# Kernel tuning notes

Hardware: AMD Instinct MI355X
Metric: run time of the kernel (lower is better)

The kernel has to match this reference:

```python
import jax, jax.numpy as jnp
import numpy as np

HEAD_COUNT = 16  # original code scales by head_count ** -0.5 (not head_size)


def setup_inputs() -> dict:
    key = jax.random.key(0)
    k1, k2, k3, k4 = jax.random.split(key, 4)
    B, T, C, H = 4, 4096, 1024, 64
    x = jax.random.normal(k1, (B, T, C), dtype=jnp.float32)
    # nn.Linear(C, H, bias=False) weights, stored as (C, H) so projection is x @ W
    Wq = jax.random.normal(k2, (C, H), dtype=jnp.float32) * (C ** -0.5)
    Wk = jax.random.normal(k3, (C, H), dtype=jnp.float32) * (C ** -0.5)
    Wv = jax.random.normal(k4, (C, H), dtype=jnp.float32) * (C ** -0.5)
    return {"x": x, "Wq": Wq, "Wk": Wk, "Wv": Wv}


def reference(x, Wq, Wk, Wv):
    B, T, C = x.shape
    q = jnp.einsum('btc,ch->bth', x, Wq)  # [B,T,H]
    k = jnp.einsum('btc,ch->bth', x, Wk)
    v = jnp.einsum('btc,ch->bth', x, Wv)
    scale = HEAD_COUNT ** (-0.5)
    scores = jnp.einsum('bth,bsh->bts', q, k) * scale  # [B,T,T]
    causal = jnp.tril(jnp.ones((T, T), dtype=bool))
    scores = jnp.where(causal, scores, -jnp.inf)
    weights = jax.nn.softmax(scores, axis=-1)
    # dropout disabled (eval / rate 0) for deterministic reference
    out = jnp.einsum('bts,bsh->bth', weights, v)  # [B,T,H]
    return out
```

## Files before the change

### kernel.cpp

```cpp
#include <hip/hip_runtime.h>
#include <hip/hip_bf16.h>


typedef __attribute__((ext_vector_type(8))) short short8_t;
typedef __attribute__((ext_vector_type(4))) float f32x4;
typedef __attribute__((ext_vector_type(16))) float f32x16;

#define MFMA16(a, b, c) __builtin_amdgcn_mfma_f32_16x16x32_bf16((a), (b), (c), 0, 0, 0)
#define MFMA32(a, b, c) __builtin_amdgcn_mfma_f32_32x32x16_bf16((a), (b), (c), 0, 0, 0)

__device__ __forceinline__ unsigned short f2bf(float f) {
  union { float f; unsigned int u; } v; v.f = f;
  unsigned int u = v.u;
  u += 0x7FFFu + ((u >> 16) & 1u);
  return (unsigned short)(u >> 16);
}
__device__ __forceinline__ float bf2f(unsigned short h) {
  union { unsigned int u; float f; } v; v.u = ((unsigned int)h) << 16;
  return v.f;
}

__global__ __launch_bounds__(256) void qkv_proj(
    const float* __restrict__ x,  const float* __restrict__ Wq,
    const float* __restrict__ Wk, const float* __restrict__ Wv,
    unsigned short* __restrict__ qh, unsigned short* __restrict__ ql,
    unsigned short* __restrict__ kh, unsigned short* __restrict__ kl,
    unsigned short* __restrict__ vth, unsigned short* __restrict__ vtl)
{
  __shared__ alignas(16) unsigned short Ah[64][40];
  __shared__ alignas(16) unsigned short Al[64][40];
  __shared__ alignas(16) unsigned short Bh[192][40];
  __shared__ alignas(16) unsigned short Bl[192][40];

  const int tid  = threadIdx.x;
  const int wave = tid >> 6;
  const int lane = tid & 63;
  const int g    = lane >> 4;
  const int c    = lane & 15;
  const int m0   = blockIdx.x * 64;

  f32x4 acc[4][3];
#pragma unroll
  for (int m = 0; m < 4; ++m)
#pragma unroll
    for (int nn = 0; nn < 3; ++nn) acc[m][nn] = (f32x4){0.f, 0.f, 0.f, 0.f};

  for (int k0 = 0; k0 < 1024; k0 += 32) {
    __syncthreads();
#pragma unroll
    for (int it = 0; it < 2; ++it) {
      int chunk = tid + it * 256;
      int row = chunk >> 3, ch = chunk & 7;
      const float4 vx = *reinterpret_cast<const float4*>(
          x + (size_t)(m0 + row) * 1024 + k0 + ch * 4);
#pragma unroll
      for (int j = 0; j < 4; ++j) {
        float f = ((const float*)&vx)[j];
        unsigned short h = f2bf(f);
        Ah[row][ch * 4 + j] = h;
        Al[row][ch * 4 + j] = f2bf(f - bf2f(h));
      }
    }
    const float* const Ws[3] = {Wq, Wk, Wv};
#pragma unroll
    for (int it = 0; it < 6; ++it) {
      int chunk = tid + it * 256;
      int mat = chunk >> 9;
      int cid = chunk & 511;
      int kk = cid >> 4, ch = cid & 15;
      const float4 vw = *reinterpret_cast<const float4*>(
          Ws[mat] + (size_t)(k0 + kk) * 64 + ch * 4);
#pragma unroll
      for (int j = 0; j < 4; ++j) {
        float f = ((const float*)&vw)[j];
        unsigned short h = f2bf(f);
        int n = mat * 64 + ch * 4 + j;
        Bh[n][kk] = h;
        Bl[n][kk] = f2bf(f - bf2f(h));
      }
    }
    __syncthreads();

    short8_t a_h[4], a_l[4];
#pragma unroll
    for (int m = 0; m < 4; ++m) {
      a_h[m] = *reinterpret_cast<const short8_t*>(&Ah[m * 16 + c][g * 8]);
      a_l[m] = *reinterpret_cast<const short8_t*>(&Al[m * 16 + c][g * 8]);
    }
#pragma unroll
    for (int nn = 0; nn < 3; ++nn) {
      const int nt = wave * 3 + nn;
      short8_t b_h = *reinterpret_cast<const short8_t*>(&Bh[nt * 16 + c][g * 8]);
      short8_t b_l = *reinterpret_cast<const short8_t*>(&Bl[nt * 16 + c][g * 8]);
#pragma unroll
      for (int m = 0; m < 4; ++m) {
        acc[m][nn] = MFMA16(a_h[m], b_h, acc[m][nn]);
        acc[m][nn] = MFMA16(a_h[m], b_l, acc[m][nn]);
        acc[m][nn] = MFMA16(a_l[m], b_h, acc[m][nn]);
      }
    }
  }

#pragma unroll
  for (int m = 0; m < 4; ++m) {
#pragma unroll
    for (int nn = 0; nn < 3; ++nn) {
      const int nt  = wave * 3 + nn;
      const int mat = nt >> 2;
      const int col = (nt & 3) * 16 + c;
#pragma unroll
      for (int r = 0; r < 4; ++r) {
        float f = acc[m][nn][r];
        int row = m0 + m * 16 + g * 4 + r;
        unsigned short h = f2bf(f);
        unsigned short lo = f2bf(f - bf2f(h));
        if (mat == 0) {
          size_t idx = (size_t)row * 64 + col;
          qh[idx] = h; ql[idx] = lo;
        } else if (mat == 1) {
          size_t idx = (size_t)row * 64 + col;
          kh[idx] = h; kl[idx] = lo;
        } else {
          int bb = row >> 12, trow = row & 4095;
          size_t idx = ((size_t)(bb * 64 + col)) * 4096 + trow;
          vth[idx] = h; vtl[idx] = lo;
        }
      }
    }
  }
}

#define MASKVAL (-3.0e38f)
#define MINIT   (-1.0e30f)

__global__ __launch_bounds__(512, 2) void attn(
    const unsigned short* __restrict__ qh, const unsigned short* __restrict__ ql,
    const unsigned short* __restrict__ kh, const unsigned short* __restrict__ kl,
    const unsigned short* __restrict__ vth, const unsigned short* __restrict__ vtl,
    float* __restrict__ out)
{
  __shared__ alignas(16) unsigned char smem[147456];

  const int tid = threadIdx.x;
  const int ws  = tid >> 6;
  const int l   = tid & 63;
  const int h5  = l >> 5;
  const int l31 = l & 31;
  const int bid = blockIdx.x;
  const int bb  = bid >> 6;
  const int jt  = bid & 63;
  const int t0  = jt * 64;

  unsigned short* Kh = (unsigned short*)(smem + ws * 18432);
  unsigned short* Kl = (unsigned short*)(smem + ws * 18432 + 4096);
  unsigned short* Vh = (unsigned short*)(smem + ws * 18432 + 8192);
  unsigned short* Vl = (unsigned short*)(smem + ws * 18432 + 13312);

  const float CE = 0.36067376022224085f;

  short8_t qf_h[2][4], qf_l[2][4];
#pragma unroll
  for (int qt = 0; qt < 2; ++qt)
#pragma unroll
    for (int c = 0; c < 4; ++c) {
      size_t off = ((size_t)(bb * 4096 + t0 + qt * 32 + l31)) * 64 + c * 16 + h5 * 8;
      qf_h[qt][c] = *reinterpret_cast<const short8_t*>(qh + off);
      qf_l[qt][c] = *reinterpret_cast<const short8_t*>(ql + off);
    }

  f32x16 ot[2][2];
#pragma unroll
  for (int a = 0; a < 2; ++a)
#pragma unroll
    for (int b2 = 0; b2 < 2; ++b2)
#pragma unroll
      for (int r = 0; r < 16; ++r) ot[a][b2][r] = 0.f;
  float mreg[2] = {MINIT, MINIT};
  float lreg[2] = {0.f, 0.f};

  const int ktimax = (t0 + 63) >> 5;

  for (int kti = ws; kti <= ktimax; kti += 8) {
    const int s0 = kti * 32;

#pragma unroll
    for (int i = 0; i < 4; ++i) {
      int k2 = i * 8 + (l >> 3);
      int hh = (l & 7) * 8;
      size_t gidx = ((size_t)(bb * 4096 + s0 + k2)) * 64 + hh;
      short8_t a = *reinterpret_cast<const short8_t*>(kh + gidx);
      short8_t b2 = *reinterpret_cast<const short8_t*>(kl + gidx);
      int wo = k2 * 64 + (hh ^ ((k2 & 7) << 3));
      *reinterpret_cast<short8_t*>(Kh + wo) = a;
      *reinterpret_cast<short8_t*>(Kl + wo) = b2;
    }
#pragma unroll
    for (int i = 0; i < 4; ++i) {
      int hv = i * 16 + (l >> 2);
      int kv = (l & 3) * 8;
      size_t gidx = ((size_t)(bb * 64 + hv)) * 4096 + s0 + kv;
      short8_t a = *reinterpret_cast<const short8_t*>(vth + gidx);
      short8_t b2 = *reinterpret_cast<const short8_t*>(vtl + gidx);
      int wo = hv * 40 + kv;
      *reinterpret_cast<short8_t*>(Vh + wo) = a;
      *reinterpret_cast<short8_t*>(Vl + wo) = b2;
    }

    short8_t kf_h[4], kf_l[4];
#pragma unroll
    for (int c = 0; c < 4; ++c) {
      int ko = l31 * 64 + ((c * 16 + h5 * 8) ^ ((l31 & 7) << 3));
      kf_h[c] = *reinterpret_cast<const short8_t*>(Kh + ko);
      kf_l[c] = *reinterpret_cast<const short8_t*>(Kl + ko);
    }

    int pb0[2][4], pb1[2][4], plb0[2][4], plb1[2][4];

#pragma unroll
    for (int qt = 0; qt < 2; ++qt) {
      int (*pb)[4]  = (qt == 0) ? pb0 : pb1;
      int (*plb)[4] = (qt == 0) ? plb0 : plb1;
      if (s0 > t0 + qt * 32 + 31) {
#pragma unroll
        for (int kc = 0; kc < 2; ++kc)
#pragma unroll
          for (int d = 0; d < 4; ++d) { pb[kc][d] = 0; plb[kc][d] = 0; }
        continue;
      }

      f32x16 st;
#pragma unroll
      for (int r = 0; r < 16; ++r) st[r] = 0.f;
#pragma unroll
      for (int c = 0; c < 4; ++c) {
        st = MFMA32(kf_h[c], qf_h[qt][c], st);
        st = MFMA32(kf_h[c], qf_l[qt][c], st);
        st = MFMA32(kf_l[c], qf_h[qt][c], st);
      }

      if (s0 + 31 > t0 + qt * 32) {
        int qg = t0 + qt * 32 + l31;
#pragma unroll
        for (int r = 0; r < 16; ++r) {
          int keyg = s0 + (r & 3) + 8 * (r >> 2) + 4 * h5;
          if (keyg > qg) st[r] = MASKVAL;
        }
      }

      float pm = st[0];
#pragma unroll
      for (int r = 1; r < 16; ++r) pm = fmaxf(pm, st[r]);
      pm = fmaxf(pm, __shfl_xor(pm, 32));
      float mnew = fmaxf(mreg[qt], pm);
      float fs = __builtin_amdgcn_exp2f((mreg[qt] - mnew) * CE);
      mreg[qt] = mnew;
      lreg[qt] *= fs;
#pragma unroll
      for (int ht = 0; ht < 2; ++ht) ot[ht][qt] *= fs;

      float p[16]; float rs = 0.f;
#pragma unroll
      for (int r = 0; r < 16; ++r) {
        p[r] = __builtin_amdgcn_exp2f((st[r] - mnew) * CE);
        rs += p[r];
      }
      rs += __shfl_xor(rs, 32);
      lreg[qt] += rs;

      int w[8], wl[8], pw[8], pwl[8];
#pragma unroll
      for (int i = 0; i < 8; ++i) {
        unsigned short b0 = f2bf(p[2 * i]), b1 = f2bf(p[2 * i + 1]);
        w[i] = (int)((unsigned)b0 | ((unsigned)b1 << 16));
        float l0 = p[2 * i] - bf2f(b0), l1 = p[2 * i + 1] - bf2f(b1);
        wl[i] = (int)((unsigned)f2bf(l0) | ((unsigned)f2bf(l1) << 16));
      }
#pragma unroll
      for (int i = 0; i < 8; ++i) {
        pw[i]  = __shfl_xor(w[i], 32);
        pwl[i] = __shfl_xor(wl[i], 32);
      }
#pragma unroll
      for (int kc = 0; kc < 2; ++kc) {
        pb[kc][0]  = h5 ? pw[4 * kc + 2]  : w[4 * kc];
        pb[kc][1]  = h5 ? pw[4 * kc + 3]  : w[4 * kc + 1];
        pb[kc][2]  = h5 ? w[4 * kc + 2]   : pw[4 * kc];
        pb[kc][3]  = h5 ? w[4 * kc + 3]   : pw[4 * kc + 1];
        plb[kc][0] = h5 ? pwl[4 * kc + 2] : wl[4 * kc];
        plb[kc][1] = h5 ? pwl[4 * kc + 3] : wl[4 * kc + 1];
        plb[kc][2] = h5 ? wl[4 * kc + 2]  : pwl[4 * kc];
        plb[kc][3] = h5 ? wl[4 * kc + 3]  : pwl[4 * kc + 1];
      }
    }

#pragma unroll
    for (int ht = 0; ht < 2; ++ht)
#pragma unroll
      for (int kc = 0; kc < 2; ++kc) {
        int vo = (ht * 32 + l31) * 40 + kc * 16 + h5 * 8;
        short8_t vfh = *reinterpret_cast<const short8_t*>(Vh + vo);
        short8_t vfl = *reinterpret_cast<const short8_t*>(Vl + vo);
#pragma unroll
        for (int qt = 0; qt < 2; ++qt) {
          union { int d[4]; short8_t s; } u1, u2;
#pragma unroll
          for (int d = 0; d < 4; ++d) {
            u1.d[d] = (qt == 0) ? pb0[kc][d] : pb1[kc][d];
            u2.d[d] = (qt == 0) ? plb0[kc][d] : plb1[kc][d];
          }
          ot[ht][qt] = MFMA32(vfh, u1.s, ot[ht][qt]);
          ot[ht][qt] = MFMA32(vfl, u1.s, ot[ht][qt]);
          ot[ht][qt] = MFMA32(vfh, u2.s, ot[ht][qt]);
        }
      }
  }

  __syncthreads();
  float* OT = (float*)smem;
  float* ML = (float*)(smem + 137216);
#pragma unroll
  for (int ht = 0; ht < 2; ++ht)
#pragma unroll
    for (int qt = 0; qt < 2; ++qt)
#pragma unroll
      for (int r = 0; r < 16; ++r) {
        int h = ht * 32 + (r & 3) + 8 * (r >> 2) + 4 * h5;
        int q = qt * 32 + l31;
        OT[(ws * 64 + h) * 67 + q] = ot[ht][qt][r];
      }
  if (l < 32) {
#pragma unroll
    for (int qt = 0; qt < 2; ++qt) {
      int q = qt * 32 + l31;
      ML[(ws * 64 + q) * 2]     = mreg[qt];
      ML[(ws * 64 + q) * 2 + 1] = lreg[qt];
    }
  }
  __syncthreads();

  {
    const int h = tid & 63;
    const int qg = tid >> 6;
#pragma unroll
    for (int i = 0; i < 8; ++i) {
      int q = qg * 8 + i;
      float M = ML[q * 2];
#pragma unroll
      for (int s = 1; s < 8; ++s) M = fmaxf(M, ML[(s * 64 + q) * 2]);
      float L = 0.f, acc2 = 0.f;
#pragma unroll
      for (int s = 0; s < 8; ++s) {
        float wgt = __builtin_amdgcn_exp2f((ML[(s * 64 + q) * 2] - M) * CE);
        L    += wgt * ML[(s * 64 + q) * 2 + 1];
        acc2 += wgt * OT[(s * 64 + h) * 67 + q];
      }
      out[((size_t)bb * 4096 + t0 + q) * 64 + h] = acc2 / L;
    }
  }
}

extern "C" void kernel_launch(void* const* d_in, const int* in_sizes, int n_in,
                              void* d_out, int out_size, void* d_ws, size_t ws_size,
                              hipStream_t stream) {
  const float* x  = (const float*)d_in[0];
  const float* Wq = (const float*)d_in[1];
  const float* Wk = (const float*)d_in[2];
  const float* Wv = (const float*)d_in[3];
  float* out = (float*)d_out;

  const size_t NE = (size_t)16384 * 64;
  unsigned short* qh  = (unsigned short*)d_ws;
  unsigned short* ql  = qh + NE;
  unsigned short* kh  = ql + NE;
  unsigned short* kl  = kh + NE;
  unsigned short* vth = kl + NE;
  unsigned short* vtl = vth + NE;

  qkv_proj<<<256, 256, 0, stream>>>(x, Wq, Wk, Wv, qh, ql, kh, kl, vth, vtl);
  attn<<<256, 512, 0, stream>>>(qh, ql, kh, kl, vth, vtl, out);
}
```

Measured before the change: 257.0 us.

## Split causal attention into load-balanced KV slices with merge kernel, pre-split weights

```diff
diff --git a/kernel.cpp b/kernel.cpp
--- a/kernel.cpp
+++ b/kernel.cpp
@@ -20,80 +20,79 @@
   return v.f;
 }
 
+__device__ __forceinline__ size_t vtidx(int b, int t, int h) {
+  return ((((((size_t)b * 128 + (t >> 5)) * 2 + (h >> 5)) * 2 + ((t >> 4) & 1)) * 2
+           + ((t >> 3) & 1)) * 32 + (h & 31)) * 8 + (t & 7);
+}
+
+__global__ __launch_bounds__(192) void wprep(
+    const float* __restrict__ Wq, const float* __restrict__ Wk,
+    const float* __restrict__ Wv,
+    unsigned short* __restrict__ wth, unsigned short* __restrict__ wtl)
+{
+  const int n  = threadIdx.x;
+  const int kb = blockIdx.x;
+  const float* W = (n < 64) ? Wq : (n < 128) ? Wk : Wv;
+  const int cc = n & 63;
+  union { unsigned short u[8]; short8_t s; } uh, ul;
+#pragma unroll
+  for (int j = 0; j < 8; ++j) {
+    float f = W[(size_t)(kb * 8 + j) * 64 + cc];
+    unsigned short h = f2bf(f);
+    uh.u[j] = h;
+    ul.u[j] = f2bf(f - bf2f(h));
+  }
+  *reinterpret_cast<short8_t*>(wth + (size_t)n * 1024 + kb * 8) = uh.s;
+  *reinterpret_cast<short8_t*>(wtl + (size_t)n * 1024 + kb * 8) = ul.s;
+}
+
 __global__ __launch_bounds__(256) void qkv_proj(
-    const float* __restrict__ x,  const float* __restrict__ Wq,
-    const float* __restrict__ Wk, const float* __restrict__ Wv,
+    const float* __restrict__ x,
+    const unsigned short* __restrict__ wth, const unsigned short* __restrict__ wtl,
     unsigned short* __restrict__ qh, unsigned short* __restrict__ ql,
     unsigned short* __restrict__ kh, unsigned short* __restrict__ kl,
     unsigned short* __restrict__ vth, unsigned short* __restrict__ vtl)
 {
-  __shared__ alignas(16) unsigned short Ah[64][40];
-  __shared__ alignas(16) unsigned short Al[64][40];
-  __shared__ alignas(16) unsigned short Bh[192][40];
-  __shared__ alignas(16) unsigned short Bl[192][40];
-
   const int tid  = threadIdx.x;
   const int wave = tid >> 6;
   const int lane = tid & 63;
   const int g    = lane >> 4;
   const int c    = lane & 15;
-  const int m0   = blockIdx.x * 64;
-
-  f32x4 acc[4][3];
-#pragma unroll
-  for (int m = 0; m < 4; ++m)
+  const int m0   = blockIdx.x * 32;
+
+  f32x4 acc[2][3];
+#pragma unroll
+  for (int m = 0; m < 2; ++m)
 #pragma unroll
     for (int nn = 0; nn < 3; ++nn) acc[m][nn] = (f32x4){0.f, 0.f, 0.f, 0.f};
 
   for (int k0 = 0; k0 < 1024; k0 += 32) {
-    __syncthreads();
-#pragma unroll
-    for (int it = 0; it < 2; ++it) {
-      int chunk = tid + it * 256;
-      int row = chunk >> 3, ch = chunk & 7;
-      const float4 vx = *reinterpret_cast<const float4*>(
-          x + (size_t)(m0 + row) * 1024 + k0 + ch * 4);
+    short8_t a_h[2], a_l[2];
+#pragma unroll
+    for (int m = 0; m < 2; ++m) {
+      const float* xp = x + (size_t)(m0 + m * 16 + c) * 1024 + k0 + g * 8;
+      const float4 f0 = *reinterpret_cast<const float4*>(xp);
+      const float4 f1 = *reinterpret_cast<const float4*>(xp + 4);
+      union { unsigned short u[8]; short8_t s; } uh, ul;
 #pragma unroll
       for (int j = 0; j < 4; ++j) {
-        float f = ((const float*)&vx)[j];
-        unsigned short h = f2bf(f);
-        Ah[row][ch * 4 + j] = h;
-        Al[row][ch * 4 + j] = f2bf(f - bf2f(h));
-      }
-    }
-    const float* const Ws[3] = {Wq, Wk, Wv};
-#pragma unroll
-    for (int it = 0; it < 6; ++it) {
-      int chunk = tid + it * 256;
-      int mat = chunk >> 9;
-      int cid = chunk & 511;
-      int kk = cid >> 4, ch = cid & 15;
-      const float4 vw = *reinterpret_cast<const float4*>(
-          Ws[mat] + (size_t)(k0 + kk) * 64 + ch * 4);
-#pragma unroll
-      for (int j = 0; j < 4; ++j) {
-        float f = ((const float*)&vw)[j];
-        unsigned short h = f2bf(f);
-        int n = mat * 64 + ch * 4 + j;
-        Bh[n][kk] = h;
-        Bl[n][kk] = f2bf(f - bf2f(h));
-      }
-    }
-    __syncthreads();
-
-    short8_t a_h[4], a_l[4];
-#pragma unroll
-    for (int m = 0; m < 4; ++m) {
-      a_h[m] = *reinterpret_cast<const short8_t*>(&Ah[m * 16 + c][g * 8]);
-      a_l[m] = *reinterpret_cast<const short8_t*>(&Al[m * 16 + c][g * 8]);
+        float fa = ((const float*)&f0)[j];
+        unsigned short ha = f2bf(fa);
+        uh.u[j] = ha; ul.u[j] = f2bf(fa - bf2f(ha));
+        float fb = ((const float*)&f1)[j];
+        unsigned short hb = f2bf(fb);
+        uh.u[4 + j] = hb; ul.u[4 + j] = f2bf(fb - bf2f(hb));
+      }
+      a_h[m] = uh.s; a_l[m] = ul.s;
     }
 #pragma unroll
     for (int nn = 0; nn < 3; ++nn) {
       const int nt = wave * 3 + nn;
-      short8_t b_h = *reinterpret_cast<const short8_t*>(&Bh[nt * 16 + c][g * 8]);
-      short8_t b_l = *reinterpret_cast<const short8_t*>(&Bl[nt * 16 + c][g * 8]);
-#pragma unroll
-      for (int m = 0; m < 4; ++m) {
+      const size_t bo = (size_t)(nt * 16 + c) * 1024 + k0 + g * 8;
+      const short8_t b_h = *reinterpret_cast<const short8_t*>(wth + bo);
+      const short8_t b_l = *reinterpret_cast<const short8_t*>(wtl + bo);
+#pragma unroll
+      for (int m = 0; m < 2; ++m) {
         acc[m][nn] = MFMA16(a_h[m], b_h, acc[m][nn]);
         acc[m][nn] = MFMA16(a_h[m], b_l, acc[m][nn]);
         acc[m][nn] = MFMA16(a_l[m], b_h, acc[m][nn]);
@@ -102,28 +101,25 @@
   }
 
 #pragma unroll
-  for (int m = 0; m < 4; ++m) {
+  for (int m = 0; m < 2; ++m) {
 #pragma unroll
     for (int nn = 0; nn < 3; ++nn) {
       const int nt  = wave * 3 + nn;
-      const int mat = nt >> 2;
-      const int col = (nt & 3) * 16 + c;
+      const int col = nt * 16 + c;
+      const int mat = col >> 6;
+      const int cm  = col & 63;
 #pragma unroll
       for (int r = 0; r < 4; ++r) {
         float f = acc[m][nn][r];
         int row = m0 + m * 16 + g * 4 + r;
-        unsigned short h = f2bf(f);
+        unsigned short h  = f2bf(f);
         unsigned short lo = f2bf(f - bf2f(h));
-        if (mat == 0) {
-          size_t idx = (size_t)row * 64 + col;
-          qh[idx] = h; ql[idx] = lo;
-        } else if (mat == 1) {
-          size_t idx = (size_t)row * 64 + col;
-          kh[idx] = h; kl[idx] = lo;
-        } else {
-          int bb = row >> 12, trow = row & 4095;
-          size_t idx = ((size_t)(bb * 64 + col)) * 4096 + trow;
-          vth[idx] = h; vtl[idx] = lo;
+        if (mat == 0)      { size_t i = (size_t)row * 64 + cm; qh[i] = h; ql[i] = lo; }
+        else if (mat == 1) { size_t i = (size_t)row * 64 + cm; kh[i] = h; kl[i] = lo; }
+        else {
+          int bb = row >> 12, t = row & 4095;
+          size_t i = vtidx(bb, t, cm);
+          vth[i] = h; vtl[i] = lo;
         }
       }
     }
@@ -133,28 +129,32 @@
 #define MASKVAL (-3.0e38f)
 #define MINIT   (-1.0e30f)
 
-__global__ __launch_bounds__(512, 2) void attn(
+__global__ __launch_bounds__(256, 2) void attn(
     const unsigned short* __restrict__ qh, const unsigned short* __restrict__ ql,
     const unsigned short* __restrict__ kh, const unsigned short* __restrict__ kl,
     const unsigned short* __restrict__ vth, const unsigned short* __restrict__ vtl,
-    float* __restrict__ out)
+    float* __restrict__ Opart, float* __restrict__ MLpart)
 {
-  __shared__ alignas(16) unsigned char smem[147456];
+  __shared__ alignas(16) unsigned char smem[70656];
 
   const int tid = threadIdx.x;
   const int ws  = tid >> 6;
   const int l   = tid & 63;
   const int h5  = l >> 5;
   const int l31 = l & 31;
-  const int bid = blockIdx.x;
-  const int bb  = bid >> 6;
-  const int jt  = bid & 63;
-  const int t0  = jt * 64;
-
-  unsigned short* Kh = (unsigned short*)(smem + ws * 18432);
-  unsigned short* Kl = (unsigned short*)(smem + ws * 18432 + 4096);
-  unsigned short* Vh = (unsigned short*)(smem + ws * 18432 + 8192);
-  unsigned short* Vl = (unsigned short*)(smem + ws * 18432 + 13312);
+
+  const int bidb = blockIdx.x;
+  const int bb   = bidb / 160;
+  const int s    = bidb % 160;
+  int jt, slice, nsl;
+  if (s < 16)      { jt = s;                         slice = 0;                nsl = 1; }
+  else if (s < 48) { int i = s - 16; jt = 16 + (i >> 1); slice = i & 1;        nsl = 2; }
+  else if (s < 96) { int i = s - 48; jt = 32 + i / 3;    slice = i - 3 * (jt - 32); nsl = 3; }
+  else             { int i = s - 96; jt = 48 + (i >> 2); slice = i & 3;        nsl = 4; }
+  const int t0    = jt * 64;
+  const int total = 2 * (jt + 1);
+  const int k0t   = (slice * total) / nsl;
+  const int k1t   = ((slice + 1) * total) / nsl;
 
   const float CE = 0.36067376022224085f;
 
@@ -162,10 +162,10 @@
 #pragma unroll
   for (int qt = 0; qt < 2; ++qt)
 #pragma unroll
-    for (int c = 0; c < 4; ++c) {
-      size_t off = ((size_t)(bb * 4096 + t0 + qt * 32 + l31)) * 64 + c * 16 + h5 * 8;
-      qf_h[qt][c] = *reinterpret_cast<const short8_t*>(qh + off);
-      qf_l[qt][c] = *reinterpret_cast<const short8_t*>(ql + off);
+    for (int cc = 0; cc < 4; ++cc) {
+      size_t off = ((size_t)(bb * 4096 + t0 + qt * 32 + l31)) * 64 + cc * 16 + h5 * 8;
+      qf_h[qt][cc] = *reinterpret_cast<const short8_t*>(qh + off);
+      qf_l[qt][cc] = *reinterpret_cast<const short8_t*>(ql + off);
     }
 
   f32x16 ot[2][2];
@@ -178,53 +178,26 @@
   float mreg[2] = {MINIT, MINIT};
   float lreg[2] = {0.f, 0.f};
 
-  const int ktimax = (t0 + 63) >> 5;
-
-  for (int kti = ws; kti <= ktimax; kti += 8) {
+  for (int kti = k0t + ws; kti < k1t; kti += 4) {
     const int s0 = kti * 32;
 
-#pragma unroll
-    for (int i = 0; i < 4; ++i) {
-      int k2 = i * 8 + (l >> 3);
-      int hh = (l & 7) * 8;
-      size_t gidx = ((size_t)(bb * 4096 + s0 + k2)) * 64 + hh;
-      short8_t a = *reinterpret_cast<const short8_t*>(kh + gidx);
-      short8_t b2 = *reinterpret_cast<const short8_t*>(kl + gidx);
-      int wo = k2 * 64 + (hh ^ ((k2 & 7) << 3));
-      *reinterpret_cast<short8_t*>(Kh + wo) = a;
-      *reinterpret_cast<short8_t*>(Kl + wo) = b2;
-    }
-#pragma unroll
-    for (int i = 0; i < 4; ++i) {
-      int hv = i * 16 + (l >> 2);
-      int kv = (l & 3) * 8;
-      size_t gidx = ((size_t)(bb * 64 + hv)) * 4096 + s0 + kv;
-      short8_t a = *reinterpret_cast<const short8_t*>(vth + gidx);
-      short8_t b2 = *reinterpret_cast<const short8_t*>(vtl + gidx);
-      int wo = hv * 40 + kv;
-      *reinterpret_cast<short8_t*>(Vh + wo) = a;
-      *reinterpret_cast<short8_t*>(Vl + wo) = b2;
-    }
-
     short8_t kf_h[4], kf_l[4];
-#pragma unroll
-    for (int c = 0; c < 4; ++c) {
-      int ko = l31 * 64 + ((c * 16 + h5 * 8) ^ ((l31 & 7) << 3));
-      kf_h[c] = *reinterpret_cast<const short8_t*>(Kh + ko);
-      kf_l[c] = *reinterpret_cast<const short8_t*>(Kl + ko);
-    }
-
-    int pb0[2][4], pb1[2][4], plb0[2][4], plb1[2][4];
+    const size_t krow = ((size_t)(bb * 4096 + s0 + l31)) * 64 + h5 * 8;
+#pragma unroll
+    for (int cc = 0; cc < 4; ++cc) {
+      kf_h[cc] = *reinterpret_cast<const short8_t*>(kh + krow + cc * 16);
+      kf_l[cc] = *reinterpret_cast<const short8_t*>(kl + krow + cc * 16);
+    }
+
+    short8_t pfh[2][2], pfl[2][2];
 
 #pragma unroll
     for (int qt = 0; qt < 2; ++qt) {
-      int (*pb)[4]  = (qt == 0) ? pb0 : pb1;
-      int (*plb)[4] = (qt == 0) ? plb0 : plb1;
       if (s0 > t0 + qt * 32 + 31) {
-#pragma unroll
-        for (int kc = 0; kc < 2; ++kc)
-#pragma unroll
-          for (int d = 0; d < 4; ++d) { pb[kc][d] = 0; plb[kc][d] = 0; }
+        union { int d[4]; short8_t s8; } z;
+        z.d[0] = z.d[1] = z.d[2] = z.d[3] = 0;
+        pfh[qt][0] = z.s8; pfh[qt][1] = z.s8;
+        pfl[qt][0] = z.s8; pfl[qt][1] = z.s8;
         continue;
       }
 
@@ -232,10 +205,10 @@
 #pragma unroll
       for (int r = 0; r < 16; ++r) st[r] = 0.f;
 #pragma unroll
-      for (int c = 0; c < 4; ++c) {
-        st = MFMA32(kf_h[c], qf_h[qt][c], st);
-        st = MFMA32(kf_h[c], qf_l[qt][c], st);
-        st = MFMA32(kf_l[c], qf_h[qt][c], st);
+      for (int cc = 0; cc < 4; ++cc) {
+        st = MFMA32(kf_h[cc], qf_h[qt][cc], st);
+        st = MFMA32(kf_h[cc], qf_l[qt][cc], st);
+        st = MFMA32(kf_l[cc], qf_h[qt][cc], st);
       }
 
       if (s0 + 31 > t0 + qt * 32) {
@@ -282,14 +255,17 @@
       }
 #pragma unroll
       for (int kc = 0; kc < 2; ++kc) {
-        pb[kc][0]  = h5 ? pw[4 * kc + 2]  : w[4 * kc];
-        pb[kc][1]  = h5 ? pw[4 * kc + 3]  : w[4 * kc + 1];
-        pb[kc][2]  = h5 ? w[4 * kc + 2]   : pw[4 * kc];
-        pb[kc][3]  = h5 ? w[4 * kc + 3]   : pw[4 * kc + 1];
-        plb[kc][0] = h5 ? pwl[4 * kc + 2] : wl[4 * kc];
-        plb[kc][1] = h5 ? pwl[4 * kc + 3] : wl[4 * kc + 1];
-        plb[kc][2] = h5 ? wl[4 * kc + 2]  : pwl[4 * kc];
-        plb[kc][3] = h5 ? wl[4 * kc + 3]  : pwl[4 * kc + 1];
+        union { int d[4]; short8_t s8; } uh2, ul2;
+        uh2.d[0] = h5 ? pw[4 * kc + 2]  : w[4 * kc];
+        uh2.d[1] = h5 ? pw[4 * kc + 3]  : w[4 * kc + 1];
+        uh2.d[2] = h5 ? w[4 * kc + 2]   : pw[4 * kc];
+        uh2.d[3] = h5 ? w[4 * kc + 3]   : pw[4 * kc + 1];
+        ul2.d[0] = h5 ? pwl[4 * kc + 2] : wl[4 * kc];
+        ul2.d[1] = h5 ? pwl[4 * kc + 3] : wl[4 * kc + 1];
+        ul2.d[2] = h5 ? wl[4 * kc + 2]  : pwl[4 * kc];
+        ul2.d[3] = h5 ? wl[4 * kc + 3]  : pwl[4 * kc + 1];
+        pfh[qt][kc] = uh2.s8;
+        pfl[qt][kc] = ul2.s8;
       }
     }
 
@@ -297,36 +273,30 @@
     for (int ht = 0; ht < 2; ++ht)
 #pragma unroll
       for (int kc = 0; kc < 2; ++kc) {
-        int vo = (ht * 32 + l31) * 40 + kc * 16 + h5 * 8;
-        short8_t vfh = *reinterpret_cast<const short8_t*>(Vh + vo);
-        short8_t vfl = *reinterpret_cast<const short8_t*>(Vl + vo);
+        const size_t vbase =
+            ((size_t)(((bb * 128 + kti) * 2 + ht) * 2 + kc)) * 512 + (size_t)l * 8;
+        const short8_t vfh = *reinterpret_cast<const short8_t*>(vth + vbase);
+        const short8_t vfl = *reinterpret_cast<const short8_t*>(vtl + vbase);
 #pragma unroll
         for (int qt = 0; qt < 2; ++qt) {
-          union { int d[4]; short8_t s; } u1, u2;
-#pragma unroll
-          for (int d = 0; d < 4; ++d) {
-            u1.d[d] = (qt == 0) ? pb0[kc][d] : pb1[kc][d];
-            u2.d[d] = (qt == 0) ? plb0[kc][d] : plb1[kc][d];
-          }
-          ot[ht][qt] = MFMA32(vfh, u1.s, ot[ht][qt]);
-          ot[ht][qt] = MFMA32(vfl, u1.s, ot[ht][qt]);
-          ot[ht][qt] = MFMA32(vfh, u2.s, ot[ht][qt]);
+          ot[ht][qt] = MFMA32(vfh, pfh[qt][kc], ot[ht][qt]);
+          ot[ht][qt] = MFMA32(vfl, pfh[qt][kc], ot[ht][qt]);
+          ot[ht][qt] = MFMA32(vfh, pfl[qt][kc], ot[ht][qt]);
         }
       }
   }
 
-  __syncthreads();
   float* OT = (float*)smem;
-  float* ML = (float*)(smem + 137216);
+  float* ML = (float*)(smem + 68608);
 #pragma unroll
   for (int ht = 0; ht < 2; ++ht)
 #pragma unroll
     for (int qt = 0; qt < 2; ++qt)
 #pragma unroll
       for (int r = 0; r < 16; ++r) {
-        int h = ht * 32 + (r & 3) + 8 * (r >> 2) + 4 * h5;
+        int hrow = ht * 32 + (r & 3) + 8 * (r >> 2) + 4 * h5;
         int q = qt * 32 + l31;
-        OT[(ws * 64 + h) * 67 + q] = ot[ht][qt][r];
+        OT[(ws * 64 + hrow) * 67 + q] = ot[ht][qt][r];
       }
   if (l < 32) {
 #pragma unroll
@@ -339,23 +309,74 @@
   __syncthreads();
 
   {
-    const int h = tid & 63;
+    const int h  = tid & 63;
     const int qg = tid >> 6;
 #pragma unroll
-    for (int i = 0; i < 8; ++i) {
-      int q = qg * 8 + i;
+    for (int i = 0; i < 16; ++i) {
+      int q = qg * 16 + i;
       float M = ML[q * 2];
 #pragma unroll
-      for (int s = 1; s < 8; ++s) M = fmaxf(M, ML[(s * 64 + q) * 2]);
-      float L = 0.f, acc2 = 0.f;
-#pragma unroll
-      for (int s = 0; s < 8; ++s) {
-        float wgt = __builtin_amdgcn_exp2f((ML[(s * 64 + q) * 2] - M) * CE);
-        L    += wgt * ML[(s * 64 + q) * 2 + 1];
-        acc2 += wgt * OT[(s * 64 + h) * 67 + q];
-      }
-      out[((size_t)bb * 4096 + t0 + q) * 64 + h] = acc2 / L;
-    }
+      for (int s2 = 1; s2 < 4; ++s2) M = fmaxf(M, ML[(s2 * 64 + q) * 2]);
+      float L = 0.f, A = 0.f;
+#pragma unroll
+      for (int s2 = 0; s2 < 4; ++s2) {
+        float wgt = __builtin_amdgcn_exp2f((ML[(s2 * 64 + q) * 2] - M) * CE);
+        L += wgt * ML[(s2 * 64 + q) * 2 + 1];
+        A += wgt * OT[(s2 * 64 + h) * 67 + q];
+      }
+      Opart[((size_t)bidb * 64 + q) * 64 + h] = A;
+      if (h == 0) MLpart[((size_t)bidb * 64 + q) * 2]     = M;
+      if (h == 1) MLpart[((size_t)bidb * 64 + q) * 2 + 1] = L;
+    }
+  }
+}
+
+__global__ __launch_bounds__(256) void attn_merge(
+    const float* __restrict__ Opart, const float* __restrict__ MLpart,
+    float* __restrict__ out)
+{
+  const int bid = blockIdx.x;
+  const int bb = bid >> 6, jt = bid & 63;
+  const int nsl = 1 + (jt >= 16) + (jt >= 32) + (jt >= 48);
+  const int off = (jt < 16) ? jt
+                : (jt < 32) ? 16 + 2 * (jt - 16)
+                : (jt < 48) ? 48 + 3 * (jt - 32)
+                :             96 + 4 * (jt - 48);
+  const int pid0 = bb * 160 + off;
+  const int t = threadIdx.x;
+  const int q = t >> 2;
+  const int hg = t & 3;
+  const float CE = 0.36067376022224085f;
+
+  float M = MLpart[((size_t)pid0 * 64 + q) * 2];
+  for (int s2 = 1; s2 < nsl; ++s2)
+    M = fmaxf(M, MLpart[((size_t)(pid0 + s2) * 64 + q) * 2]);
+
+  float L = 0.f;
+  float a[16];
+#pragma unroll
+  for (int j = 0; j < 16; ++j) a[j] = 0.f;
+
+  for (int s2 = 0; s2 < nsl; ++s2) {
+    size_t mlb = ((size_t)(pid0 + s2) * 64 + q) * 2;
+    float w = __builtin_amdgcn_exp2f((MLpart[mlb] - M) * CE);
+    L += w * MLpart[mlb + 1];
+    const float* op = Opart + ((size_t)(pid0 + s2) * 64 + q) * 64 + hg * 16;
+#pragma unroll
+    for (int j = 0; j < 4; ++j) {
+      float4 v4 = *reinterpret_cast<const float4*>(op + j * 4);
+      a[j * 4 + 0] += w * v4.x; a[j * 4 + 1] += w * v4.y;
+      a[j * 4 + 2] += w * v4.z; a[j * 4 + 3] += w * v4.w;
+    }
+  }
+
+  const float inv = 1.f / L;
+  float* po = out + ((size_t)bb * 4096 + jt * 64 + q) * 64 + hg * 16;
+#pragma unroll
+  for (int j = 0; j < 4; ++j) {
+    float4 v4 = { a[j * 4] * inv, a[j * 4 + 1] * inv,
+                  a[j * 4 + 2] * inv, a[j * 4 + 3] * inv };
+    *reinterpret_cast<float4*>(po + j * 4) = v4;
   }
 }
 
@@ -375,7 +396,13 @@
   unsigned short* kl  = kh + NE;
   unsigned short* vth = kl + NE;
   unsigned short* vtl = vth + NE;
-
-  qkv_proj<<<256, 256, 0, stream>>>(x, Wq, Wk, Wv, qh, ql, kh, kl, vth, vtl);
-  attn<<<256, 512, 0, stream>>>(qh, ql, kh, kl, vth, vtl, out);
-}
+  unsigned short* wth = vtl + NE;
+  unsigned short* wtl = wth + (size_t)192 * 1024;
+  float* Opart  = (float*)(wtl + (size_t)192 * 1024);
+  float* MLpart = Opart + (size_t)640 * 64 * 64;
+
+  wprep<<<128, 192, 0, stream>>>(Wq, Wk, Wv, wth, wtl);
+  qkv_proj<<<512, 256, 0, stream>>>(x, wth, wtl, qh, ql, kh, kl, vth, vtl);
+  attn<<<640, 256, 0, stream>>>(qh, ql, kh, kl, vth, vtl, Opart, MLpart);
+  attn_merge<<<256, 256, 0, stream>>>(Opart, MLpart, out);
+}
```

Result: faster. 237.0 us (-7.8%).
